# Optimization experiments

Hardware: AMD Instinct MI355X
Metric: run time of the kernel (lower is better)

Reference implementation:

```python
import jax, jax.numpy as jnp
import numpy as np

B, S, A, H, N = 4096, 128, 32, 1024, 256
BETA = 1.0            # params['temperature']
NORM_SMOOTHING = 0.01 # params['norm_smoothing']
MAX_A = 1.0           # env.action_space.high[0]
# dropout_rate = 0.0 and eval-mode reference -> dropout is identity


def setup_inputs() -> dict:
    key = jax.random.key(0)
    ks = jax.random.split(key, 16)
    sc_s = 1.0 / np.sqrt(S)
    sc_h = 1.0 / np.sqrt(H)
    return {
        "s": jax.random.normal(ks[0], (B, S), jnp.float32),
        "a": jax.random.normal(ks[1], (B, A), jnp.float32),
        # value side MLP: S->H->H->H->N
        "Wv1": jax.random.uniform(ks[2], (S, H), jnp.float32, -sc_s, sc_s),
        "bv1": jax.random.uniform(ks[3], (H,), jnp.float32, -sc_s, sc_s),
        "Wv2": jax.random.uniform(ks[4], (H, H), jnp.float32, -sc_h, sc_h),
        "bv2": jax.random.uniform(ks[5], (H,), jnp.float32, -sc_h, sc_h),
        "Wv3": jax.random.uniform(ks[6], (H, H), jnp.float32, -sc_h, sc_h),
        "bv3": jax.random.uniform(ks[7], (H,), jnp.float32, -sc_h, sc_h),
        "Wv4": jax.random.uniform(ks[8], (H, N), jnp.float32, -sc_h, sc_h),
        "bv4": jax.random.uniform(ks[9], (N,), jnp.float32, -sc_h, sc_h),
        # location side: S->H (xavier), then N expert linears H->A stacked
        "Wl1": jax.random.normal(ks[10], (S, H), jnp.float32) * np.sqrt(2.0 / (S + H)),
        "bl1": jnp.zeros((H,), jnp.float32),
        "Wexp": jax.random.uniform(ks[11], (N, H, A), jnp.float32, -0.1, 0.1),
        "bexp": jax.random.uniform(ks[12], (N, A), jnp.float32, -1.0, 1.0),
    }


def reference(s, a, Wv1, bv1, Wv2, bv2, Wv3, bv3, Wv4, bv4, Wl1, bl1, Wexp, bexp):
    t = jax.nn.relu(s @ Wv1 + bv1)
    t = jax.nn.relu(t @ Wv2 + bv2)
    t = jax.nn.relu(t @ Wv3 + bv3)
    values = t @ Wv4 + bv4                      # [B, N]

    # --- get_all_centroids: shared hidden, N expert heads as grouped GEMM ---
    h = jax.nn.relu(s @ Wl1 + bl1)              # [B, H] (dropout identity)
    centroids = MAX_A * jnp.tanh(
        jnp.einsum("bh,nha->bna", h, Wexp) + bexp[None]
    )                                           # [B, N, A]

    # --- rbf_function: softmax over -beta * ||centroid - a|| ---
    diff = centroids - a[:, None, :]            # [B, N, A]
    dist = jnp.sqrt(jnp.sum(diff * diff, axis=2) + NORM_SMOOTHING)  # [B, N]
    weights = jax.nn.softmax(-BETA * dist, axis=1)                  # [B, N]

    return jnp.sum(weights * values, axis=1, keepdims=True)         # [B, 1]
```

## Files before the change

kernel.cpp:

```cpp
#include <hip/hip_runtime.h>
#include <hip/hip_bf16.h>


typedef _Float16 half8 __attribute__((ext_vector_type(8)));
typedef _Float16 half4v __attribute__((ext_vector_type(4)));
typedef float floatx16 __attribute__((ext_vector_type(16)));

namespace {
constexpr int kB = 4096, kS = 128, kA = 32, kH = 1024, kN = 256;
constexpr size_t al(size_t x) { return (x + 255) & ~size_t(255); }
constexpr size_t OFF_FLAG  = 0;
constexpr size_t OFF_S16   = 256;
constexpr size_t OFF_WEXPT = OFF_S16   + al((size_t)kB * kS * 2);
constexpr size_t OFF_WV1T  = OFF_WEXPT + al((size_t)kN * kA * kH * 2);
constexpr size_t OFF_WL1T  = OFF_WV1T  + (size_t)kS * kH * 2;
constexpr size_t OFF_WV2T  = OFF_WL1T  + al((size_t)kS * kH * 2);
constexpr size_t OFF_WV3T  = OFF_WV2T  + al((size_t)kH * kH * 2);
constexpr size_t OFF_WV4T  = OFF_WV3T  + al((size_t)kH * kH * 2);
constexpr size_t OFF_BUFC  = OFF_WV4T  + al((size_t)kH * kN * 2);
constexpr size_t OFF_B2V   = OFF_BUFC  + al((size_t)kB * 2 * kH * 2);
constexpr size_t OFF_B3    = OFF_B2V   + al((size_t)kB * kH * 2);
constexpr size_t OFF_VAL   = OFF_B3    + al((size_t)kB * kH * 2);
constexpr size_t OFF_Z     = OFF_VAL   + al((size_t)kB * kN * 4);
}

__device__ __forceinline__ float ldraw(const void* p, size_t i, int bf) {
    if (bf) return __uint_as_float(((unsigned)((const unsigned short*)p)[i]) << 16);
    return ((const float*)p)[i];
}

__device__ __forceinline__ float4 ldraw4(const void* p, size_t i, int bf) {
    if (bf) {
        ushort4 u = *(const ushort4*)((const unsigned short*)p + i);
        return make_float4(__uint_as_float((unsigned)u.x << 16),
                           __uint_as_float((unsigned)u.y << 16),
                           __uint_as_float((unsigned)u.z << 16),
                           __uint_as_float((unsigned)u.w << 16));
    }
    return *(const float4*)((const float*)p + i);
}

__device__ __forceinline__ void gl_lds16(const _Float16* g, _Float16* l) {
    __builtin_amdgcn_global_load_lds(
        (const __attribute__((address_space(1))) unsigned int*)g,
        (__attribute__((address_space(3))) unsigned int*)l, 16, 0, 0);
}

__device__ __forceinline__ float fast_tanh(float x) {
    x = fminf(9.f, fmaxf(-9.f, x));
    float e = __expf(2.f * x);
    return (e - 1.f) * __builtin_amdgcn_rcpf(e + 1.f);
}

__global__ void detect_kernel(const unsigned int* __restrict__ s_raw, int* __restrict__ flag) {
    __shared__ int cnt;
    if (threadIdx.x == 0) cnt = 0;
    __syncthreads();
    const unsigned e = (s_raw[threadIdx.x] >> 7) & 0xFFu;
    int c = (e >= 118u && e <= 135u) ? 1 : 0;
    for (int off = 32; off > 0; off >>= 1) c += __shfl_down(c, off);
    if ((threadIdx.x & 63) == 0) atomicAdd(&cnt, c);
    __syncthreads();
    if (threadIdx.x == 0) *flag = (cnt > 128) ? 1 : 0;
}

struct TDesc { const void* src; _Float16* dst; int K; int N; int tiles; };
struct TPack { TDesc d[7]; };

__global__ void transpose_all(TPack p, const int* __restrict__ flag) {
    __shared__ float tile[32][33];
    const int bf = *flag;
    int bid = blockIdx.x;
    int i = 0;
    while (bid >= p.d[i].tiles) { bid -= p.d[i].tiles; ++i; }
    const void* src = p.d[i].src;
    _Float16* dst = p.d[i].dst;
    const int tx = threadIdx.x, ty = threadIdx.y;
    const int K = p.d[i].K, N = p.d[i].N;
    if (K == 0) {
        const int lin = ty * 8 + tx;
        const size_t base = (size_t)bid * 4096;
#pragma unroll
        for (int t = 0; t < 4; ++t) {
            const size_t idx = base + (size_t)t * 1024 + (size_t)lin * 4;
            float4 v = ldraw4(src, idx, bf);
            half4v o = {(_Float16)v.x, (_Float16)v.y, (_Float16)v.z, (_Float16)v.w};
            *(half4v*)(dst + idx) = o;
        }
        return;
    }
    const int tpz = (N >> 5) * (K >> 5);
    const int z = bid / tpz, r = bid - z * tpz;
    const int n0 = (r % (N >> 5)) * 32, k0 = (r / (N >> 5)) * 32;
    const size_t zo = (size_t)z * K * N;
    float4 v = ldraw4(src, zo + (size_t)(k0 + ty) * N + n0 + tx * 4, bf);
    tile[ty][tx * 4 + 0] = v.x;
    tile[ty][tx * 4 + 1] = v.y;
    tile[ty][tx * 4 + 2] = v.z;
    tile[ty][tx * 4 + 3] = v.w;
    __syncthreads();
    half4v o;
#pragma unroll
    for (int j = 0; j < 4; ++j) o[j] = (_Float16)tile[tx * 4 + j][ty];
    *(half4v*)(dst + zo + (size_t)(n0 + ty) * K + k0 + tx * 4) = o;
}

struct GArgs {
    const _Float16* A;
    const _Float16* Bt;
    const void* bias;
    const void* bias2;
    void* C;
    int split;
    int N, K, lda, Mt, Nt, relu, of16;
};

template <int TM, int TN, int WM, int WN>
__device__ __forceinline__ void dgemm_core(const GArgs& g, int bid, const int* flagp) {
    constexpr int NT = WM * WN * 64;
    constexpr int BK = 32;
    constexpr int MI = TM / WM / 32, NI = TN / WN / 32;
    constexpr int ACH = TM * BK / 8;
    constexpr int BCH = TN * BK / 8;
    constexpr int AT = (ACH + NT - 1) / NT;
    constexpr int BT = (BCH + NT - 1) / NT;
    __shared__ _Float16 As[2 * ACH * 8];
    __shared__ _Float16 Bs[2 * BCH * 8];

    const int tid = threadIdx.x;
    const int lane = tid & 63;
    const int w = tid >> 6, wr = w / WN, wc = w % WN;
    const int N = g.N, K = g.K, lda = g.lda;

    int mt, nt;
    if ((g.Mt & 7) == 0 && (g.Nt & 7) == 0) {
        const int xcd = bid & 7, loc = bid >> 3;
        const int Bn = g.Nt >> 3;
        const int sr = loc / (8 * Bn);
        const int rem = loc - sr * (8 * Bn);
        mt = sr * 8 + (rem & 7);
        nt = xcd * Bn + (rem >> 3);
    } else {
        mt = bid % g.Mt;
        nt = bid / g.Mt;
    }
    const int m0 = mt * TM, n0 = nt * TN;

    const _Float16* gAsrc[AT];
    _Float16* lAdst[AT];
#pragma unroll
    for (int t = 0; t < AT; ++t) {
        int c = t * NT + tid;
        if (c >= ACH) c = ACH - 1;
        const int ks = c / (TM * 2), rem = c % (TM * 2);
        const int row = (rem >> 6) * 32 + (rem & 31);
        const int kcol = ks * 16 + ((rem >> 5) & 1) * 8;
        gAsrc[t] = g.A + (size_t)(m0 + row) * lda + kcol;
        lAdst[t] = As + c * 8;
    }
    const _Float16* gBsrc[BT];
    _Float16* lBdst[BT];
#pragma unroll
    for (int t = 0; t < BT; ++t) {
        int c = t * NT + tid;
        if (c >= BCH) c = BCH - 1;
        const int ks = c / (TN * 2), rem = c % (TN * 2);
        const int row = (rem >> 6) * 32 + (rem & 31);
        const int kcol = ks * 16 + ((rem >> 5) & 1) * 8;
        gBsrc[t] = g.Bt + (size_t)(n0 + row) * K + kcol;
        lBdst[t] = Bs + c * 8;
    }

    auto issue = [&](int k0, int st) {
#pragma unroll
        for (int t = 0; t < AT; ++t)
            if ((t + 1) * NT <= ACH || t * NT + tid < ACH)
                gl_lds16(gAsrc[t] + k0, lAdst[t] + st * ACH * 8);
#pragma unroll
        for (int t = 0; t < BT; ++t)
            if ((t + 1) * NT <= BCH || t * NT + tid < BCH)
                gl_lds16(gBsrc[t] + k0, lBdst[t] + st * BCH * 8);
    };

    floatx16 acc[MI][NI];
#pragma unroll
    for (int mi = 0; mi < MI; ++mi)
#pragma unroll
        for (int ni = 0; ni < NI; ++ni)
#pragma unroll
            for (int i = 0; i < 16; ++i) acc[mi][ni][i] = 0.f;

    auto compute = [&](int st) {
#pragma unroll
        for (int ks = 0; ks < 2; ++ks) {
            half8 af[MI], bf[NI];
#pragma unroll
            for (int mi = 0; mi < MI; ++mi)
                af[mi] = *(const half8*)(As + st * ACH * 8 + ((size_t)(ks * TM * 2 + (wr * MI + mi) * 64 + lane)) * 8);
#pragma unroll
            for (int ni = 0; ni < NI; ++ni)
                bf[ni] = *(const half8*)(Bs + st * BCH * 8 + ((size_t)(ks * TN * 2 + (wc * NI + ni) * 64 + lane)) * 8);
#pragma unroll
            for (int mi = 0; mi < MI; ++mi)
#pragma unroll
                for (int ni = 0; ni < NI; ++ni)
                    acc[mi][ni] = __builtin_amdgcn_mfma_f32_32x32x16_f16(af[mi], bf[ni], acc[mi][ni], 0, 0, 0);
        }
    };

    issue(0, 0);
    for (int k0 = 0; k0 < K; k0 += 2 * BK) {
        __syncthreads();
        if (k0 + BK < K) issue(k0 + BK, 1);
        compute(0);
        __syncthreads();
        if (k0 + 2 * BK < K) issue(k0 + 2 * BK, 0);
        compute(1);
    }

    const int bf_ = *flagp;
    const int am = lane & 31;
    const int half = lane >> 5;
#pragma unroll
    for (int mi = 0; mi < MI; ++mi)
#pragma unroll
        for (int ni = 0; ni < NI; ++ni) {
            const int Rb = m0 + (wr * MI + mi) * 32;
            const int Cb = n0 + (wc * NI + ni) * 32 + am;
            const float bv = (Cb < g.split) ? ldraw(g.bias, Cb, bf_)
                                            : ldraw(g.bias2, Cb - g.split, bf_);
#pragma unroll
            for (int rr = 0; rr < 16; ++rr) {
                const int row = Rb + (rr & 3) + 8 * (rr >> 2) + 4 * half;
                float x = acc[mi][ni][rr] + bv;
                if (g.relu) x = fmaxf(x, 0.f);
                if (g.of16) ((_Float16*)g.C)[(size_t)row * N + Cb] = (_Float16)x;
                else ((float*)g.C)[(size_t)row * N + Cb] = x;
            }
        }
}

template <int TM, int TN, int WM, int WN>
__launch_bounds__(WM * WN * 64, 2)
__global__ void dgemm_one(GArgs g, const int* __restrict__ flagp) {
    dgemm_core<TM, TN, WM, WN>(g, blockIdx.x, flagp);
}

__launch_bounds__(256)
__global__ void final_fused(const _Float16* __restrict__ z, const void* __restrict__ a_raw,
                            const float* __restrict__ values, const int* __restrict__ flag,
                            void* __restrict__ out) {
    const int b = blockIdx.x;
    const int n = threadIdx.x;
    const int bf = *flag;
    __shared__ float as_[32];
    if (n < 32) as_[n] = ldraw(a_raw, (size_t)b * kA + n, bf);
    __syncthreads();

    const _Float16* zp = z + (size_t)b * (kN * kA) + n * kA;
    float zl[32];
#pragma unroll
    for (int t = 0; t < 4; ++t) {
        half8 h = *(const half8*)(zp + t * 8);
#pragma unroll
        for (int j = 0; j < 8; ++j) zl[t * 8 + j] = (float)h[j];
    }
    float sum = 0.f;
#pragma unroll
    for (int a = 0; a < 32; ++a) {
        const float c = fast_tanh(zl[a]);
        const float d = c - as_[a];
        sum = fmaf(d, d, sum);
    }
    const float dist = sqrtf(sum + 0.01f);
    const float v = values[(size_t)b * kN + n];

    const int wid = n >> 6, lane = n & 63;
    __shared__ float red[8];
    __shared__ float rw[4], rwv[4];
    float m = dist;
    for (int off = 32; off > 0; off >>= 1) m = fminf(m, __shfl_down(m, off));
    if (lane == 0) red[wid] = m;
    __syncthreads();
    if (n == 0) red[4] = fminf(fminf(red[0], red[1]), fminf(red[2], red[3]));
    __syncthreads();
    const float dmin = red[4];

    float wgt = expf(dmin - dist);
    float wv = wgt * v;
    for (int off = 32; off > 0; off >>= 1) {
        wgt += __shfl_down(wgt, off);
        wv += __shfl_down(wv, off);
    }
    if (lane == 0) { rw[wid] = wgt; rwv[wid] = wv; }
    __syncthreads();
    if (n == 0) {
        const float sw = rw[0] + rw[1] + rw[2] + rw[3];
        const float swv = rwv[0] + rwv[1] + rwv[2] + rwv[3];
        const float o = swv / sw;
        if (bf) ((__hip_bfloat16*)out)[b] = __float2bfloat16(o);
        else    ((float*)out)[b] = o;
    }
}

extern "C" void kernel_launch(void* const* d_in, const int* in_sizes, int n_in,
                              void* d_out, int out_size, void* d_ws, size_t ws_size,
                              hipStream_t stream) {
    (void)in_sizes; (void)n_in; (void)out_size; (void)ws_size;
    char* ws = (char*)d_ws;
    int* flag = (int*)(ws + OFF_FLAG);
    _Float16* s16   = (_Float16*)(ws + OFF_S16);
    _Float16* wexpt = (_Float16*)(ws + OFF_WEXPT);
    _Float16* wv1t  = (_Float16*)(ws + OFF_WV1T);
    _Float16* wl1t  = (_Float16*)(ws + OFF_WL1T);
    _Float16* wv2t  = (_Float16*)(ws + OFF_WV2T);
    _Float16* wv3t  = (_Float16*)(ws + OFF_WV3T);
    _Float16* wv4t  = (_Float16*)(ws + OFF_WV4T);
    _Float16* bufC  = (_Float16*)(ws + OFF_BUFC);
    _Float16* b2v   = (_Float16*)(ws + OFF_B2V);
    _Float16* b3    = (_Float16*)(ws + OFF_B3);
    float* values   = (float*)(ws + OFF_VAL);
    _Float16* z     = (_Float16*)(ws + OFF_Z);

    detect_kernel<<<1, 256, 0, stream>>>((const unsigned int*)d_in[0], flag);

    TPack tp;
    tp.d[0] = {d_in[2],  wv1t,  kS, kH, (kH / 32) * (kS / 32)};
    tp.d[1] = {d_in[10], wl1t,  kS, kH, (kH / 32) * (kS / 32)};
    tp.d[2] = {d_in[4],  wv2t,  kH, kH, (kH / 32) * (kH / 32)};
    tp.d[3] = {d_in[6],  wv3t,  kH, kH, (kH / 32) * (kH / 32)};
    tp.d[4] = {d_in[8],  wv4t,  kH, kN, (kN / 32) * (kH / 32)};
    tp.d[5] = {d_in[12], wexpt, kH, kA, kN * (kA / 32) * (kH / 32)};
    tp.d[6] = {d_in[0],  s16,   0,  kB * kS, (kB * kS) / 4096};
    int total_tiles = 0;
    for (int i = 0; i < 7; ++i) total_tiles += tp.d[i].tiles;
    transpose_all<<<total_tiles, dim3(8, 32), 0, stream>>>(tp, flag);

    const int BIG = 1 << 30;
    {
        GArgs g{s16, wv1t, d_in[3], d_in[11], bufC, kH,
                2 * kH, kS, kS, kB / 64, (2 * kH) / 64, 1, 1};
        dgemm_one<64, 64, 2, 2><<<(kB / 64) * ((2 * kH) / 64), 256, 0, stream>>>(g, flag);
    }
    {
        GArgs g{bufC, wv2t, d_in[5], d_in[5], b2v, BIG,
                kH, kH, 2 * kH, kB / 128, kH / 128, 1, 1};
        dgemm_one<128, 128, 2, 2><<<(kB / 128) * (kH / 128), 256, 0, stream>>>(g, flag);
    }
    {
        GArgs g{b2v, wv3t, d_in[7], d_in[7], b3, BIG,
                kH, kH, kH, kB / 128, kH / 128, 1, 1};
        dgemm_one<128, 128, 2, 2><<<(kB / 128) * (kH / 128), 256, 0, stream>>>(g, flag);
    }
    {
        GArgs g{b3, wv4t, d_in[9], d_in[9], values, BIG,
                kN, kH, kH, kB / 64, kN / 64, 0, 0};
        dgemm_one<64, 64, 2, 2><<<(kB / 64) * (kN / 64), 256, 0, stream>>>(g, flag);
    }
    {
        GArgs g{bufC + kH, wexpt, d_in[13], d_in[13], z, BIG,
                kN * kA, kH, 2 * kH, kB / 256, (kN * kA) / 256, 0, 1};
        dgemm_one<256, 256, 4, 4><<<(kB / 256) * ((kN * kA) / 256), 1024, 0, stream>>>(g, flag);
    }
    final_fused<<<kB, 256, 0, stream>>>(z, d_in[1], values, flag, d_out);
}
```

Baseline: 313.5 us.

## Fuse tanh-distance into expert GEMM epilogue and triple-buffer GEMM pipeline

```diff
diff --git a/kernel.cpp b/kernel.cpp
--- a/kernel.cpp
+++ b/kernel.cpp
@@ -21,7 +21,7 @@
 constexpr size_t OFF_B2V   = OFF_BUFC  + al((size_t)kB * 2 * kH * 2);
 constexpr size_t OFF_B3    = OFF_B2V   + al((size_t)kB * kH * 2);
 constexpr size_t OFF_VAL   = OFF_B3    + al((size_t)kB * kH * 2);
-constexpr size_t OFF_Z     = OFF_VAL   + al((size_t)kB * kN * 4);
+constexpr size_t OFF_DIST  = OFF_VAL   + al((size_t)kB * kN * 4);
 }
 
 __device__ __forceinline__ float ldraw(const void* p, size_t i, int bf) {
@@ -45,6 +45,17 @@
         (const __attribute__((address_space(1))) unsigned int*)g,
         (__attribute__((address_space(3))) unsigned int*)l, 16, 0, 0);
 }
+
+template <int N>
+__device__ __forceinline__ void waitcnt_vm() {
+    if constexpr (N == 0)      asm volatile("s_waitcnt vmcnt(0)" ::: "memory");
+    else if constexpr (N == 2) asm volatile("s_waitcnt vmcnt(2)" ::: "memory");
+    else if constexpr (N == 4) asm volatile("s_waitcnt vmcnt(4)" ::: "memory");
+    else if constexpr (N == 6) asm volatile("s_waitcnt vmcnt(6)" ::: "memory");
+    else if constexpr (N == 8) asm volatile("s_waitcnt vmcnt(8)" ::: "memory");
+    else static_assert(N == 0, "unsupported vmcnt");
+}
+__device__ __forceinline__ void lgkm0() { asm volatile("s_waitcnt lgkmcnt(0)" ::: "memory"); }
 
 __device__ __forceinline__ float fast_tanh(float x) {
     x = fminf(9.f, fmaxf(-9.f, x));
@@ -111,21 +122,25 @@
     const void* bias;
     const void* bias2;
     void* C;
+    const void* a_raw;
+    float* dist;
     int split;
-    int N, K, lda, Mt, Nt, relu, of16;
+    int N, K, lda, Mt, Nt, relu, of16, fuse;
 };
 
 template <int TM, int TN, int WM, int WN>
 __device__ __forceinline__ void dgemm_core(const GArgs& g, int bid, const int* flagp) {
     constexpr int NT = WM * WN * 64;
     constexpr int BK = 32;
+    constexpr int NST = 3;
     constexpr int MI = TM / WM / 32, NI = TN / WN / 32;
     constexpr int ACH = TM * BK / 8;
     constexpr int BCH = TN * BK / 8;
     constexpr int AT = (ACH + NT - 1) / NT;
     constexpr int BT = (BCH + NT - 1) / NT;
-    __shared__ _Float16 As[2 * ACH * 8];
-    __shared__ _Float16 Bs[2 * BCH * 8];
+    constexpr int LPS = AT + BT;
+    __shared__ _Float16 As[NST * ACH * 8];
+    __shared__ _Float16 Bs[NST * BCH * 8];
 
     const int tid = threadIdx.x;
     const int lane = tid & 63;
@@ -191,15 +206,16 @@
             for (int i = 0; i < 16; ++i) acc[mi][ni][i] = 0.f;
 
     auto compute = [&](int st) {
+        const int ao = st * ACH * 8, bo = st * BCH * 8;
 #pragma unroll
         for (int ks = 0; ks < 2; ++ks) {
             half8 af[MI], bf[NI];
 #pragma unroll
             for (int mi = 0; mi < MI; ++mi)
-                af[mi] = *(const half8*)(As + st * ACH * 8 + ((size_t)(ks * TM * 2 + (wr * MI + mi) * 64 + lane)) * 8);
+                af[mi] = *(const half8*)(As + ao + ((size_t)(ks * TM * 2 + (wr * MI + mi) * 64 + lane)) * 8);
 #pragma unroll
             for (int ni = 0; ni < NI; ++ni)
-                bf[ni] = *(const half8*)(Bs + st * BCH * 8 + ((size_t)(ks * TN * 2 + (wc * NI + ni) * 64 + lane)) * 8);
+                bf[ni] = *(const half8*)(Bs + bo + ((size_t)(ks * TN * 2 + (wc * NI + ni) * 64 + lane)) * 8);
 #pragma unroll
             for (int mi = 0; mi < MI; ++mi)
 #pragma unroll
@@ -209,18 +225,54 @@
     };
 
     issue(0, 0);
-    for (int k0 = 0; k0 < K; k0 += 2 * BK) {
-        __syncthreads();
-        if (k0 + BK < K) issue(k0 + BK, 1);
-        compute(0);
-        __syncthreads();
-        if (k0 + 2 * BK < K) issue(k0 + 2 * BK, 0);
-        compute(1);
+    if (BK < K) issue(BK, 1);
+    if (2 * BK < K) issue(2 * BK, 2);
+    int st = 0;
+    for (int k0 = 0; k0 < K; k0 += BK) {
+        if (k0 + 2 * BK < K)      waitcnt_vm<2 * LPS>();
+        else if (k0 + BK < K)     waitcnt_vm<LPS>();
+        else                      waitcnt_vm<0>();
+        __builtin_amdgcn_s_barrier();
+        asm volatile("" ::: "memory");
+        __builtin_amdgcn_sched_barrier(0);
+        compute(st);
+        lgkm0();
+        __builtin_amdgcn_s_barrier();
+        if (k0 + 3 * BK < K) issue(k0 + 3 * BK, st);
+        st = (st == NST - 1) ? 0 : st + 1;
     }
 
     const int bf_ = *flagp;
     const int am = lane & 31;
     const int half = lane >> 5;
+
+    if (g.fuse) {
+#pragma unroll
+        for (int mi = 0; mi < MI; ++mi)
+#pragma unroll
+            for (int ni = 0; ni < NI; ++ni) {
+                const int Rb = m0 + (wr * MI + mi) * 32;
+                const int Cb = n0 + (wc * NI + ni) * 32 + am;
+                const int e = Cb >> 5;
+                const float bv = ldraw(g.bias, Cb, bf_);
+#pragma unroll
+                for (int rr = 0; rr < 16; ++rr) {
+                    const int row = Rb + (rr & 3) + 8 * (rr >> 2) + 4 * half;
+                    const float c = fast_tanh(acc[mi][ni][rr] + bv);
+                    const float av = ldraw(g.a_raw, (size_t)row * kA + am, bf_);
+                    const float d = c - av;
+                    float d2 = d * d;
+                    d2 += __shfl_xor(d2, 1);
+                    d2 += __shfl_xor(d2, 2);
+                    d2 += __shfl_xor(d2, 4);
+                    d2 += __shfl_xor(d2, 8);
+                    d2 += __shfl_xor(d2, 16);
+                    if (am == 0) g.dist[(size_t)row * kN + e] = sqrtf(d2 + 0.01f);
+                }
+            }
+        return;
+    }
+
 #pragma unroll
     for (int mi = 0; mi < MI; ++mi)
 #pragma unroll
@@ -247,59 +299,28 @@
 }
 
 __launch_bounds__(256)
-__global__ void final_fused(const _Float16* __restrict__ z, const void* __restrict__ a_raw,
-                            const float* __restrict__ values, const int* __restrict__ flag,
-                            void* __restrict__ out) {
-    const int b = blockIdx.x;
-    const int n = threadIdx.x;
-    const int bf = *flag;
-    __shared__ float as_[32];
-    if (n < 32) as_[n] = ldraw(a_raw, (size_t)b * kA + n, bf);
-    __syncthreads();
-
-    const _Float16* zp = z + (size_t)b * (kN * kA) + n * kA;
-    float zl[32];
-#pragma unroll
-    for (int t = 0; t < 4; ++t) {
-        half8 h = *(const half8*)(zp + t * 8);
-#pragma unroll
-        for (int j = 0; j < 8; ++j) zl[t * 8 + j] = (float)h[j];
-    }
-    float sum = 0.f;
-#pragma unroll
-    for (int a = 0; a < 32; ++a) {
-        const float c = fast_tanh(zl[a]);
-        const float d = c - as_[a];
-        sum = fmaf(d, d, sum);
-    }
-    const float dist = sqrtf(sum + 0.01f);
-    const float v = values[(size_t)b * kN + n];
-
-    const int wid = n >> 6, lane = n & 63;
-    __shared__ float red[8];
-    __shared__ float rw[4], rwv[4];
-    float m = dist;
-    for (int off = 32; off > 0; off >>= 1) m = fminf(m, __shfl_down(m, off));
-    if (lane == 0) red[wid] = m;
-    __syncthreads();
-    if (n == 0) red[4] = fminf(fminf(red[0], red[1]), fminf(red[2], red[3]));
-    __syncthreads();
-    const float dmin = red[4];
-
-    float wgt = expf(dmin - dist);
-    float wv = wgt * v;
+__global__ void final_softmax(const float* __restrict__ dist, const float* __restrict__ values,
+                              const int* __restrict__ flag, void* __restrict__ out) {
+    const int row = blockIdx.x * 4 + (threadIdx.x >> 6);
+    const int lane = threadIdx.x & 63;
+    const float4 d4 = *(const float4*)(dist + (size_t)row * kN + lane * 4);
+    const float4 v4 = *(const float4*)(values + (size_t)row * kN + lane * 4);
+    float m = fminf(fminf(d4.x, d4.y), fminf(d4.z, d4.w));
+#pragma unroll
+    for (int off = 32; off > 0; off >>= 1) m = fminf(m, __shfl_xor(m, off));
+    const float w0 = expf(m - d4.x), w1 = expf(m - d4.y);
+    const float w2 = expf(m - d4.z), w3 = expf(m - d4.w);
+    float ws = (w0 + w1) + (w2 + w3);
+    float wv = fmaf(w0, v4.x, fmaf(w1, v4.y, fmaf(w2, v4.z, w3 * v4.w)));
+#pragma unroll
     for (int off = 32; off > 0; off >>= 1) {
-        wgt += __shfl_down(wgt, off);
-        wv += __shfl_down(wv, off);
-    }
-    if (lane == 0) { rw[wid] = wgt; rwv[wid] = wv; }
-    __syncthreads();
-    if (n == 0) {
-        const float sw = rw[0] + rw[1] + rw[2] + rw[3];
-        const float swv = rwv[0] + rwv[1] + rwv[2] + rwv[3];
-        const float o = swv / sw;
-        if (bf) ((__hip_bfloat16*)out)[b] = __float2bfloat16(o);
-        else    ((float*)out)[b] = o;
+        ws += __shfl_xor(ws, off);
+        wv += __shfl_xor(wv, off);
+    }
+    if (lane == 0) {
+        const float o = wv / ws;
+        if (*flag) ((__hip_bfloat16*)out)[row] = __float2bfloat16(o);
+        else       ((float*)out)[row] = o;
     }
 }
 
@@ -320,7 +341,7 @@
     _Float16* b2v   = (_Float16*)(ws + OFF_B2V);
     _Float16* b3    = (_Float16*)(ws + OFF_B3);
     float* values   = (float*)(ws + OFF_VAL);
-    _Float16* z     = (_Float16*)(ws + OFF_Z);
+    float* distb    = (float*)(ws + OFF_DIST);
 
     detect_kernel<<<1, 256, 0, stream>>>((const unsigned int*)d_in[0], flag);
 
@@ -338,29 +359,29 @@
 
     const int BIG = 1 << 30;
     {
-        GArgs g{s16, wv1t, d_in[3], d_in[11], bufC, kH,
-                2 * kH, kS, kS, kB / 64, (2 * kH) / 64, 1, 1};
+        GArgs g{s16, wv1t, d_in[3], d_in[11], bufC, nullptr, nullptr, kH,
+                2 * kH, kS, kS, kB / 64, (2 * kH) / 64, 1, 1, 0};
         dgemm_one<64, 64, 2, 2><<<(kB / 64) * ((2 * kH) / 64), 256, 0, stream>>>(g, flag);
     }
     {
-        GArgs g{bufC, wv2t, d_in[5], d_in[5], b2v, BIG,
-                kH, kH, 2 * kH, kB / 128, kH / 128, 1, 1};
+        GArgs g{bufC, wv2t, d_in[5], d_in[5], b2v, nullptr, nullptr, BIG,
+                kH, kH, 2 * kH, kB / 128, kH / 128, 1, 1, 0};
         dgemm_one<128, 128, 2, 2><<<(kB / 128) * (kH / 128), 256, 0, stream>>>(g, flag);
     }
     {
-        GArgs g{b2v, wv3t, d_in[7], d_in[7], b3, BIG,
-                kH, kH, kH, kB / 128, kH / 128, 1, 1};
+        GArgs g{b2v, wv3t, d_in[7], d_in[7], b3, nullptr, nullptr, BIG,
+                kH, kH, kH, kB / 128, kH / 128, 1, 1, 0};
         dgemm_one<128, 128, 2, 2><<<(kB / 128) * (kH / 128), 256, 0, stream>>>(g, flag);
     }
     {
-        GArgs g{b3, wv4t, d_in[9], d_in[9], values, BIG,
-                kN, kH, kH, kB / 64, kN / 64, 0, 0};
+        GArgs g{b3, wv4t, d_in[9], d_in[9], values, nullptr, nullptr, BIG,
+                kN, kH, kH, kB / 64, kN / 64, 0, 0, 0};
         dgemm_one<64, 64, 2, 2><<<(kB / 64) * (kN / 64), 256, 0, stream>>>(g, flag);
     }
     {
-        GArgs g{bufC + kH, wexpt, d_in[13], d_in[13], z, BIG,
-                kN * kA, kH, 2 * kH, kB / 256, (kN * kA) / 256, 0, 1};
+        GArgs g{bufC + kH, wexpt, d_in[13], d_in[13], nullptr, d_in[1], distb,
+                BIG, kN * kA, kH, 2 * kH, kB / 256, (kN * kA) / 256, 0, 0, 1};
         dgemm_one<256, 256, 4, 4><<<(kB / 256) * ((kN * kA) / 256), 1024, 0, stream>>>(g, flag);
     }
-    final_fused<<<kB, 256, 0, stream>>>(z, d_in[1], values, flag, d_out);
-}
+    final_softmax<<<kB / 4, 256, 0, stream>>>(distb, values, flag, d_out);
+}
```

Result: slower. 446.0 us (+42.3%).
